# Optimization experiments

Hardware: AMD Instinct MI355X
Metric: run time of the kernel (lower is better)

The kernel has to match this reference:

```python
import jax, jax.numpy as jnp
import numpy as np

B, T_ENC, ENC_H = 32, 512, 512
H, E, V, STEPS = 512, 512, 32000, 64
EOS_IDX = 2


def setup_inputs() -> dict:
    key = jax.random.key(0)
    ks = jax.random.split(key, 20)
    s = 0.05
    inp = {
        "encoder_outputs": jax.random.normal(ks[0], (B, T_ENC, ENC_H), jnp.float32),
        "enc_h": jax.random.normal(ks[1], (1, B, ENC_H), jnp.float32),
        "enc_c": jax.random.normal(ks[2], (1, B, ENC_H), jnp.float32),
        "trg_var": jax.random.randint(ks[3], (B, STEPS), 0, V),
        "max_length": STEPS,
        # learned parameters
        "embedding": jax.random.normal(ks[4], (V, E), jnp.float32) * s,
        "Wa": jax.random.normal(ks[5], (T_ENC, E + H), jnp.float32) * s,   # attn: Linear(E+H -> T)
        "ba": jnp.zeros((T_ENC,), jnp.float32),
        "Wc": jax.random.normal(ks[6], (E, E + ENC_H), jnp.float32) * s,   # attn_combine
        "bc": jnp.zeros((E,), jnp.float32),
        "Wh0": jax.random.normal(ks[7], (H, ENC_H), jnp.float32) * s,      # enc_to_dec_h0 (no bias)
        "Wc0": jax.random.normal(ks[8], (H, ENC_H), jnp.float32) * s,      # enc_to_dec_c0 (no bias)
        "Wih": jax.random.normal(ks[9], (4 * H, E), jnp.float32) * s,      # LSTM input weights (i,f,g,o)
        "Whh": jax.random.normal(ks[10], (4 * H, H), jnp.float32) * s,
        "bih": jnp.zeros((4 * H,), jnp.float32),
        "bhh": jnp.zeros((4 * H,), jnp.float32),
        "Wp": jax.random.normal(ks[11], (H, E), jnp.float32) * s,          # pre_output_layer
        "bp": jnp.zeros((H,), jnp.float32),
        "Wo": jax.random.normal(ks[12], (V, H), jnp.float32) * s,          # output_layer
        "bo": jnp.zeros((V,), jnp.float32),
    }
    return inp


def _decode(encoder_outputs, enc_h, enc_c, embedding, Wa, ba, Wc, bc, Wh0, Wc0,
            Wih, Whh, bih, bhh, Wp, bp, Wo, bo, trg_var, max_length):
    # init hidden from encoder final state (pass_hidden_state, LSTM, 1 layer)
    h0 = enc_h[0] @ Wh0.T  # (B,H)
    c0 = enc_c[0] @ Wc0.T
    mask0 = jnp.ones((trg_var.shape[0],), bool)

    # teacher forcing: input embedding at step 0 is zeros, then emb(trg[:, i-1])
    emb_trg = embedding[trg_var[:, :max_length - 1]]          # (B,S-1,E)
    emb_seq = jnp.concatenate(
        [jnp.zeros((1,) + (trg_var.shape[0], embedding.shape[1]), embedding.dtype),
         jnp.transpose(emb_trg, (1, 0, 2))], axis=0)          # (S,B,E)

    def step(carry, emb_prev):
        h, c, mask = carry
        # Bahdanau-style location attention over encoder positions
        aw = jax.nn.softmax(jnp.concatenate([emb_prev, h], -1) @ Wa.T + ba, axis=-1)  # (B,T)
        ctx = jnp.einsum('bt,bte->be', aw, encoder_outputs)                            # (B,encH)
        comb = jax.nn.relu(jnp.concatenate([emb_prev, ctx], -1) @ Wc.T + bc)           # (B,E)
        # LSTM cell (PyTorch gate order i,f,g,o)
        gates = comb @ Wih.T + bih + h @ Whh.T + bhh
        i_, f_, g_, o_ = jnp.split(gates, 4, axis=-1)
        c = jax.nn.sigmoid(f_) * c + jax.nn.sigmoid(i_) * jnp.tanh(g_)
        h = jax.nn.sigmoid(o_) * jnp.tanh(c)
        # use_prev_word=False, use_dec_state=False -> predict from attn-combined output
        pre = comb @ Wp.T + bp                                                          # (B,H)
        lp = jax.nn.log_softmax(pre @ Wo.T + bo, axis=-1)                               # (B,V)
        pred = jnp.argmax(lp, axis=-1)
        mask_out = mask                       # masks are appended before the EOS update
        new_mask = (pred != EOS_IDX) & mask
        return (h, c, new_mask), (lp, pred, h, mask_out)

    (_, _, _), (lps, preds, states, masks) = jax.lax.scan(step, (h0, c0, mask0), emb_seq)
    return (jnp.transpose(lps, (1, 0, 2)),       # log_probs (B,S,V)
            preds.T,                              # preds (B,S)
            jnp.transpose(states, (1, 0, 2)),     # decoder states (B,S,H)
            masks.T.astype(jnp.int32))            # mask (B,S)


def reference(encoder_outputs, enc_h, enc_c, trg_var, max_length, embedding, Wa, ba,
              Wc, bc, Wh0, Wc0, Wih, Whh, bih, bhh, Wp, bp, Wo, bo):
    return _decode(encoder_outputs, enc_h, enc_c, embedding, Wa, ba, Wc, bc, Wh0, Wc0,
                   Wih, Whh, bih, bhh, Wp, bp, Wo, bo, trg_var, max_length)
```

## Files before the change

### kernel.cpp

```cpp
#include <hip/hip_runtime.h>


#define NEGF (-3.4028235e38f)

typedef short bf8 __attribute__((ext_vector_type(8)));
typedef unsigned short us8 __attribute__((ext_vector_type(8)));
typedef float f32x4 __attribute__((ext_vector_type(4)));

static __device__ __forceinline__ float sigf(float x) { return 1.0f / (1.0f + expf(-x)); }

static __device__ __forceinline__ float aload(const float* p) {
    return __hip_atomic_load(p, __ATOMIC_RELAXED, __HIP_MEMORY_SCOPE_AGENT);
}
static __device__ __forceinline__ void astore(float* p, float v) {
    __hip_atomic_store(p, v, __ATOMIC_RELAXED, __HIP_MEMORY_SCOPE_AGENT);
}
static __device__ __forceinline__ unsigned fordkey(float f) {
    unsigned u = __float_as_uint(f);
    return (u & 0x80000000u) ? ~u : (u | 0x80000000u);
}
static __device__ __forceinline__ unsigned short f2bf(float x) {
    unsigned u = __float_as_uint(x);
    return (unsigned short)((u + 0x7FFFu + ((u >> 16) & 1u)) >> 16);
}
static __device__ __forceinline__ float bf2f(unsigned short b) {
    return __uint_as_float(((unsigned)b) << 16);
}

static __device__ __forceinline__ void bar_arrive(unsigned* ctr) {
    __syncthreads();
    if (threadIdx.x == 0) {
        asm volatile("s_waitcnt vmcnt(0)" ::: "memory");
        __hip_atomic_fetch_add(ctr, 1u, __ATOMIC_RELAXED, __HIP_MEMORY_SCOPE_AGENT);
    }
}
static __device__ __forceinline__ void bar_wait(unsigned* ctr, unsigned target) {
    if (threadIdx.x == 0) {
        while ((int)(__hip_atomic_load(ctr, __ATOMIC_RELAXED, __HIP_MEMORY_SCOPE_AGENT)
                     - target) < 0) {
            __builtin_amdgcn_s_sleep(1);
        }
    }
    __syncthreads();
}

__global__ __launch_bounds__(256) void k_transpose(const float* __restrict__ src,
    float* __restrict__ dst, int rows, int cols, int ld, int coff)
{
    __shared__ float tile[32][33];
    int c0 = blockIdx.x * 32, r0 = blockIdx.y * 32;
    int tx = threadIdx.x & 31, ty = threadIdx.x >> 5;
#pragma unroll
    for (int i = 0; i < 32; i += 8)
        tile[ty + i][tx] = src[(size_t)(r0 + ty + i) * ld + coff + c0 + tx];
    __syncthreads();
#pragma unroll
    for (int i = 0; i < 32; i += 8)
        dst[(size_t)(c0 + ty + i) * rows + r0 + tx] = tile[tx][ty + i];
}

__global__ __launch_bounds__(512) void k_init_state(const float* __restrict__ vec,
    const float* __restrict__ W, float* __restrict__ dst, float* __restrict__ dstT)
{
    int b = blockIdx.x, j = threadIdx.x;
    __shared__ float sv[512];
    sv[j] = vec[b * 512 + j];
    __syncthreads();
    const float* wr = W + (size_t)j * 512;
    float a0 = 0, a1 = 0, a2 = 0, a3 = 0;
#pragma unroll 4
    for (int k = 0; k < 512; k += 4) {
        float4 w = *reinterpret_cast<const float4*>(wr + k);
        a0 += sv[k] * w.x; a1 += sv[k + 1] * w.y;
        a2 += sv[k + 2] * w.z; a3 += sv[k + 3] * w.w;
    }
    float v = (a0 + a1) + (a2 + a3);
    if (dst) dst[b * 512 + j] = v;
    dstT[j * 32 + b] = v;
}

__global__ __launch_bounds__(256) void k_gather(const int* __restrict__ trg,
    const float* __restrict__ emb, float* __restrict__ eseq)
{
    int gid = blockIdx.x * 256 + threadIdx.x;
    int m = gid >> 7, e4 = gid & 127;
    int t = m >> 5, b = m & 31;
    float4 v = make_float4(0.f, 0.f, 0.f, 0.f);
    if (t > 0) {
        int row = trg[b * 64 + (t - 1)];
        v = *reinterpret_cast<const float4*>(emb + (size_t)row * 512 + e4 * 4);
    }
    *reinterpret_cast<float4*>(eseq + (size_t)m * 512 + e4 * 4) = v;
}

__global__ __launch_bounds__(256) void k_gemm_nt(const float* __restrict__ A, int lda,
    size_t strideA, const float* __restrict__ B, int ldb, const float* __restrict__ bias,
    float* __restrict__ C, size_t strideC, int N, int K)
{
    __shared__ float sA[32][260];
    __shared__ float sB[32][132];
    A += strideA * blockIdx.z;
    C += strideC * blockIdx.z;
    int tid = threadIdx.x;
    int m0 = blockIdx.x * 256, n0 = blockIdx.y * 128;
    int tx = tid & 15, ty = tid >> 4;
    float acc[16][8] = {};
    for (int k0 = 0; k0 < K; k0 += 32) {
#pragma unroll
        for (int i = 0; i < 8; ++i) {
            int f4 = tid + i * 256;
            int r = f4 >> 3, c4 = f4 & 7;
            float4 va = *reinterpret_cast<const float4*>(A + (size_t)(m0 + r) * lda + k0 + c4 * 4);
            sA[c4 * 4 + 0][r] = va.x; sA[c4 * 4 + 1][r] = va.y;
            sA[c4 * 4 + 2][r] = va.z; sA[c4 * 4 + 3][r] = va.w;
        }
#pragma unroll
        for (int i = 0; i < 4; ++i) {
            int f4 = tid + i * 256;
            int r = f4 >> 3, c4 = f4 & 7;
            float4 vb = *reinterpret_cast<const float4*>(B + (size_t)(n0 + r) * ldb + k0 + c4 * 4);
            sB[c4 * 4 + 0][r] = vb.x; sB[c4 * 4 + 1][r] = vb.y;
            sB[c4 * 4 + 2][r] = vb.z; sB[c4 * 4 + 3][r] = vb.w;
        }
        __syncthreads();
#pragma unroll 4
        for (int k = 0; k < 32; ++k) {
            float a[16], b[8];
            *reinterpret_cast<float4*>(&a[0])  = *reinterpret_cast<const float4*>(&sA[k][ty * 16]);
            *reinterpret_cast<float4*>(&a[4])  = *reinterpret_cast<const float4*>(&sA[k][ty * 16 + 4]);
            *reinterpret_cast<float4*>(&a[8])  = *reinterpret_cast<const float4*>(&sA[k][ty * 16 + 8]);
            *reinterpret_cast<float4*>(&a[12]) = *reinterpret_cast<const float4*>(&sA[k][ty * 16 + 12]);
            *reinterpret_cast<float4*>(&b[0]) = *reinterpret_cast<const float4*>(&sB[k][tx * 8]);
            *reinterpret_cast<float4*>(&b[4]) = *reinterpret_cast<const float4*>(&sB[k][tx * 8 + 4]);
#pragma unroll
            for (int i = 0; i < 16; ++i)
#pragma unroll
                for (int j = 0; j < 8; ++j)
                    acc[i][j] += a[i] * b[j];
        }
        __syncthreads();
    }
#pragma unroll
    for (int i = 0; i < 16; ++i) {
        int row = m0 + ty * 16 + i;
        float* cp = C + (size_t)row * N + n0 + tx * 8;
        float v[8];
#pragma unroll
        for (int j = 0; j < 8; ++j) v[j] = acc[i][j];
        if (bias) {
            const float* bb = bias + n0 + tx * 8;
#pragma unroll
            for (int j = 0; j < 8; ++j) v[j] += bb[j];
        }
        *reinterpret_cast<float4*>(cp) = make_float4(v[0], v[1], v[2], v[3]);
        *reinterpret_cast<float4*>(cp + 4) = make_float4(v[4], v[5], v[6], v[7]);
    }
}

__global__ __launch_bounds__(256) void k_splitA(const float* __restrict__ pre,
    unsigned short* __restrict__ Asp)
{
    int idx = blockIdx.x * 256 + threadIdx.x;
    int m = idx >> 9, k = idx & 511;
    float x = pre[(size_t)m * 512 + k];
    unsigned short h = f2bf(x);
    unsigned short lo = f2bf(x - bf2f(h));
    unsigned short* ap = Asp + (size_t)m * 1024 + k;
    ap[0] = h; ap[512] = lo;
}

__global__ __launch_bounds__(256) void k_mfma(
    const unsigned short* __restrict__ Asp,
    const float* __restrict__ Wo,
    const float* __restrict__ bo,
    float* __restrict__ out0,
    unsigned long long* __restrict__ keyr, float* __restrict__ sumr)
{
    __shared__ unsigned short sAb[2][128 * 64];
    __shared__ unsigned short sBb[128 * 64];
    int tid = threadIdx.x;
    int m0 = blockIdx.x * 128, n0 = blockIdx.y * 128;
    int l = tid & 63, wv = tid >> 6;
    int wr = wv >> 1, wc = wv & 1;
    int lm = l & 15, lg = l >> 4;

    f32x4 acc[4][4] = {};

    for (int kb = 0; kb < 8; ++kb) {
#pragma unroll
        for (int i = 0; i < 8; ++i) {
            int p = tid + i * 256;
            int seg = p >> 10;
            int q2 = p & 1023;
            int row = q2 >> 3, pk = q2 & 7;
            int widx = row * 64 + ((pk * 8) ^ ((row & 7) << 3));
            *reinterpret_cast<us8*>(&sAb[seg][widx]) =
                *reinterpret_cast<const us8*>(
                    Asp + (size_t)(m0 + row) * 1024 + seg * 512 + kb * 64 + pk * 8);
        }
#pragma unroll
        for (int i = 0; i < 4; ++i) {
            int p = tid + i * 256;
            int row = p >> 3, pk = p & 7;
            int widx = row * 64 + ((pk * 8) ^ ((row & 7) << 3));
            const float* bp = Wo + (size_t)(n0 + row) * 512 + kb * 64 + pk * 8;
            float4 b0 = *reinterpret_cast<const float4*>(bp);
            float4 b1 = *reinterpret_cast<const float4*>(bp + 4);
            unsigned short hw[8] = { f2bf(b0.x), f2bf(b0.y), f2bf(b0.z), f2bf(b0.w),
                                     f2bf(b1.x), f2bf(b1.y), f2bf(b1.z), f2bf(b1.w) };
            *reinterpret_cast<us8*>(&sBb[widx]) = *reinterpret_cast<const us8*>(hw);
        }
        __syncthreads();
#pragma unroll
        for (int ks = 0; ks < 2; ++ks) {
            bf8 bfr[4];
#pragma unroll
            for (int fc = 0; fc < 4; ++fc) {
                int row = wc * 64 + fc * 16 + lm;
                int idx = row * 64 + ((ks * 32 + lg * 8) ^ ((row & 7) << 3));
                bfr[fc] = *reinterpret_cast<const bf8*>(&sBb[idx]);
            }
#pragma unroll
            for (int aseg = 0; aseg < 2; ++aseg) {
                bf8 af[4];
#pragma unroll
                for (int fr = 0; fr < 4; ++fr) {
                    int row = wr * 64 + fr * 16 + lm;
                    int idx = row * 64 + ((ks * 32 + lg * 8) ^ ((row & 7) << 3));
                    af[fr] = *reinterpret_cast<const bf8*>(&sAb[aseg][idx]);
                }
#pragma unroll
                for (int fr = 0; fr < 4; ++fr)
#pragma unroll
                    for (int fc = 0; fc < 4; ++fc)
                        acc[fr][fc] = __builtin_amdgcn_mfma_f32_16x16x32_bf16(
                            af[fr], bfr[fc], acc[fr][fc], 0, 0, 0);
            }
        }
        __syncthreads();
    }

#pragma unroll
    for (int fr = 0; fr < 4; ++fr) {
#pragma unroll
        for (int j = 0; j < 4; ++j) {
            int m = m0 + wr * 64 + fr * 16 + lg * 4 + j;
            size_t crow = (size_t)((m & 31) * 64 + (m >> 5));
            float* cp = out0 + crow * 32000 + n0 + wc * 64 + lm;
            float vv[4];
            float mval = NEGF; int midx = 0; float esum = 0.f;
#pragma unroll
            for (int fc = 0; fc < 4; ++fc) {
                int col = n0 + wc * 64 + fc * 16 + lm;
                float v = acc[fr][fc][j] + bo[col];
                vv[fc] = v;
                if (v > mval) { mval = v; midx = col; }
                esum += expf(v);
            }
#pragma unroll
            for (int fc = 0; fc < 4; ++fc) cp[fc * 16] = vv[fc];
#pragma unroll
            for (int msk = 1; msk <= 8; msk <<= 1) {
                float vo = __shfl_xor(mval, msk);
                int   io = __shfl_xor(midx, msk);
                float so = __shfl_xor(esum, msk);
                esum += so;
                if (vo > mval || (vo == mval && io < midx)) { mval = vo; midx = io; }
            }
            if (lm == 0) {
                unsigned long long key =
                    ((unsigned long long)fordkey(mval) << 32) | (unsigned)(~(unsigned)midx);
                atomicMax(&keyr[crow], key);
                atomicAdd(&sumr[crow], esum);
            }
        }
    }
}

__global__ __launch_bounds__(1024) void k_fused(
    const float* __restrict__ WaT, const float* __restrict__ zemb,
    const float* __restrict__ cemb, const float* __restrict__ encWc,
    const float* __restrict__ Wih, const float* __restrict__ Whh,
    const float* __restrict__ bih, const float* __restrict__ bhh,
    float* __restrict__ h_g, const float* __restrict__ cT,
    float* __restrict__ z_g, float* __restrict__ combS,
    float* __restrict__ comb_g, float* __restrict__ states,
    unsigned* __restrict__ bar)
{
    __shared__ float eW[512][64];
    __shared__ float hsh[512];
    __shared__ float csh[512];
    __shared__ float zl[512];
    __shared__ float red16[16][64];
    __shared__ float wred[8];
    __shared__ float wred2[8];
    __shared__ float sgate[4][64];
    __shared__ float carr[64];

    int tid = threadIdx.x, bid = blockIdx.x;
    int b = bid >> 3, s = bid & 7;
    int jj = tid & 63, q = tid >> 6;
    unsigned* barb = bar + b * 32;
    unsigned nbar = 0;

    int wv = tid >> 6, lane = tid & 63;
    int rowid = wv * 16 + (lane >> 2);
    int g = rowid >> 6, jgl = rowid & 63;
    int kq = lane & 3;
    const float* whp = Whh + (size_t)(g * 512 + s * 64 + jgl) * 512;
    const float* wip = Wih + (size_t)(g * 512 + s * 64 + jgl) * 512;

    {
        const float* src = encWc + ((size_t)b << 18) + s * 64;
        for (int i = tid; i < 512 * 16; i += 1024) {
            int t = i >> 4, c4 = i & 15;
            float4 v = *reinterpret_cast<const float4*>(src + (size_t)t * 512 + c4 * 4);
            *reinterpret_cast<float4*>(&eW[t][c4 * 4]) = v;
        }
    }
    if (tid < 64) carr[tid] = cT[(s * 64 + tid) * 32 + b];

    for (int tstep = 0; tstep < 64; ++tstep) {
        if (tid < 512) hsh[tid] = aload(h_g + b * 512 + tid);
        __syncthreads();
        {
            float acc = 0.f;
            const float* hp = hsh + q * 32;
            const float* wp = WaT + (size_t)(q * 32) * 512 + s * 64 + jj;
#pragma unroll 8
            for (int k = 0; k < 32; ++k)
                acc += hp[k] * wp[(size_t)k * 512];
            red16[q][jj] = acc;
        }
        __syncthreads();
        if (tid < 64) {
            float v = 0.f;
#pragma unroll
            for (int r = 0; r < 16; ++r) v += red16[r][jj];
            v += zemb[((size_t)tstep * 32 + b) * 512 + s * 64 + jj];
            astore(z_g + b * 512 + s * 64 + jj, v);
        }
        ++nbar; bar_arrive(barb);

        float acc_hh = 0.f;
#pragma unroll 8
        for (int i = 0; i < 32; ++i) {
            int k = kq * 4 + i * 16;
            float4 v4 = *reinterpret_cast<const float4*>(whp + k);
            acc_hh += v4.x * hsh[k]     + v4.y * hsh[k + 1]
                    + v4.z * hsh[k + 2] + v4.w * hsh[k + 3];
        }
        bar_wait(barb, nbar * 8u);

        {
            float zv = 0.f;
            if (tid < 512) {
                zv = aload(z_g + b * 512 + tid);
                float m = zv;
#pragma unroll
                for (int o = 32; o > 0; o >>= 1) m = fmaxf(m, __shfl_xor(m, o));
                if ((tid & 63) == 0) wred[tid >> 6] = m;
            }
            __syncthreads();
            float mx = fmaxf(fmaxf(fmaxf(wred[0], wred[1]), fmaxf(wred[2], wred[3])),
                             fmaxf(fmaxf(wred[4], wred[5]), fmaxf(wred[6], wred[7])));
            if (tid < 512) {
                float e = expf(zv - mx);
                zl[tid] = e;
                float sm = e;
#pragma unroll
                for (int o = 32; o > 0; o >>= 1) sm += __shfl_xor(sm, o);
                if ((tid & 63) == 0) wred2[tid >> 6] = sm;
            }
            __syncthreads();
            float ssum = ((wred2[0] + wred2[1]) + (wred2[2] + wred2[3]))
                       + ((wred2[4] + wred2[5]) + (wred2[6] + wred2[7]));
            float inv = 1.0f / ssum;

            float acc = 0.f;
#pragma unroll 8
            for (int i = 0; i < 32; ++i)
                acc += zl[q * 32 + i] * eW[q * 32 + i][jj];
            red16[q][jj] = acc;
            __syncthreads();
            if (tid < 64) {
                float v = 0.f;
#pragma unroll
                for (int r = 0; r < 16; ++r) v += red16[r][jj];
                v = v * inv + cemb[((size_t)tstep * 32 + b) * 512 + s * 64 + jj];
                v = fmaxf(v, 0.f);
                comb_g[((size_t)tstep * 32 + b) * 512 + s * 64 + jj] = v;
                astore(combS + b * 512 + s * 64 + jj, v);
            }
        }
        ++nbar; bar_arrive(barb); bar_wait(barb, nbar * 8u);

        if (tid < 512) csh[tid] = aload(combS + b * 512 + tid);
        __syncthreads();
        {
            float acc = acc_hh;
#pragma unroll 8
            for (int i = 0; i < 32; ++i) {
                int k = kq * 4 + i * 16;
                float4 w4 = *reinterpret_cast<const float4*>(wip + k);
                acc += w4.x * csh[k]     + w4.y * csh[k + 1]
                     + w4.z * csh[k + 2] + w4.w * csh[k + 3];
            }
            acc += __shfl_xor(acc, 1);
            acc += __shfl_xor(acc, 2);
            if (kq == 0) sgate[g][jgl] = acc;
        }
        __syncthreads();
        if (tid < 64) {
            int jg = s * 64 + tid;
            float gi = sgate[0][tid] + bih[jg] + bhh[jg];
            float gf = sgate[1][tid] + bih[512 + jg] + bhh[512 + jg];
            float gg = sgate[2][tid] + bih[1024 + jg] + bhh[1024 + jg];
            float go = sgate[3][tid] + bih[1536 + jg] + bhh[1536 + jg];
            float c = carr[tid];
            float cn = sigf(gf) * c + sigf(gi) * tanhf(gg);
            float hn = sigf(go) * tanhf(cn);
            carr[tid] = cn;
            astore(h_g + b * 512 + jg, hn);
            states[((size_t)b * 64 + tstep) * 512 + jg] = hn;
        }
        ++nbar; bar_arrive(barb); bar_wait(barb, nbar * 8u);
    }
}

__global__ __launch_bounds__(1024) void k_stepA(
    const float* __restrict__ WaT, const float* __restrict__ zemb_t,
    const float* __restrict__ cemb_t, const float* __restrict__ encWc,
    const float* __restrict__ h_g, float* __restrict__ comb_t,
    float* __restrict__ combT)
{
    int b = blockIdx.x, tid = threadIdx.x;
    int j = tid & 511, kh = tid >> 9;
    __shared__ float sh[512];
    __shared__ float zp[2][512];
    __shared__ float p[512];
    __shared__ float red[16];
    __shared__ float red2[16];

    if (tid < 512) sh[tid] = h_g[b * 512 + tid];
    __syncthreads();
    {
        float acc = 0.f;
        const float* hp = sh + kh * 256;
        const float* wp = WaT + (size_t)(kh * 256) * 512 + j;
#pragma unroll 4
        for (int k = 0; k < 256; ++k) acc += hp[k] * wp[(size_t)k * 512];
        zp[kh][j] = acc;
    }
    __syncthreads();
    float zv = 0.f;
    if (tid < 512) zv = zp[0][tid] + zp[1][tid] + zemb_t[b * 512 + tid];
    float m = (tid < 512) ? zv : NEGF;
#pragma unroll
    for (int o = 32; o > 0; o >>= 1) m = fmaxf(m, __shfl_xor(m, o));
    if ((tid & 63) == 0) red[tid >> 6] = m;
    __syncthreads();
    float mx = red[0];
#pragma unroll
    for (int w = 1; w < 16; ++w) mx = fmaxf(mx, red[w]);
    float e = (tid < 512) ? expf(zv - mx) : 0.f;
    float sm = e;
#pragma unroll
    for (int o = 32; o > 0; o >>= 1) sm += __shfl_xor(sm, o);
    if ((tid & 63) == 0) red2[tid >> 6] = sm;
    __syncthreads();
    float S = 0.f;
#pragma unroll
    for (int w = 0; w < 16; ++w) S += red2[w];
    if (tid < 512) p[tid] = e * (1.0f / S);
    __syncthreads();
    {
        float acc = 0.f;
        const float* pp = p + kh * 256;
        const float* ep = encWc + ((size_t)b << 18) + (size_t)(kh * 256) * 512 + j;
#pragma unroll 4
        for (int k = 0; k < 256; ++k) acc += pp[k] * ep[(size_t)k * 512];
        zp[kh][j] = acc;
    }
    __syncthreads();
    if (tid < 512) {
        float v = zp[0][tid] + zp[1][tid] + cemb_t[b * 512 + tid];
        v = fmaxf(v, 0.f);
        comb_t[b * 512 + tid] = v;
        combT[tid * 32 + b] = v;
    }
}

__global__ __launch_bounds__(512) void k_stepB(
    const float* __restrict__ Wih, const float* __restrict__ Whh,
    const float* __restrict__ bih, const float* __restrict__ bhh,
    const float* __restrict__ combT, const float* __restrict__ hTr,
    float* __restrict__ hTw, float* __restrict__ cT, float* __restrict__ h_g,
    float* __restrict__ states, int tstep)
{
    __shared__ float sg2[2][2][4][32];
    int tid = threadIdx.x, bid = blockIdx.x;
    {
        int bb = tid & 31, g = (tid >> 5) & 3, hf = (tid >> 7) & 1, j2 = tid >> 8;
        int jg = bid * 2 + j2;
        int grow = g * 512 + jg;
        const float* wi = Wih + (size_t)grow * 512 + hf * 256;
        const float* wh = Whh + (size_t)grow * 512 + hf * 256;
        const float* cb = combT + (size_t)hf * 256 * 32 + bb;
        const float* hb = hTr + (size_t)hf * 256 * 32 + bb;
        float acc = 0.f;
#pragma unroll 4
        for (int k4 = 0; k4 < 64; ++k4) {
            float4 wi4 = *reinterpret_cast<const float4*>(wi + k4 * 4);
            float4 wh4 = *reinterpret_cast<const float4*>(wh + k4 * 4);
            acc += wi4.x * cb[(k4 * 4 + 0) * 32] + wh4.x * hb[(k4 * 4 + 0) * 32];
            acc += wi4.y * cb[(k4 * 4 + 1) * 32] + wh4.y * hb[(k4 * 4 + 1) * 32];
            acc += wi4.z * cb[(k4 * 4 + 2) * 32] + wh4.z * hb[(k4 * 4 + 2) * 32];
            acc += wi4.w * cb[(k4 * 4 + 3) * 32] + wh4.w * hb[(k4 * 4 + 3) * 32];
        }
        sg2[hf][j2][g][bb] = acc;
    }
    __syncthreads();
    if (tid < 64) {
        int bb = tid & 31, j2 = tid >> 5;
        int jg = bid * 2 + j2;
        float gi = sg2[0][j2][0][bb] + sg2[1][j2][0][bb] + bih[jg] + bhh[jg];
        float gf = sg2[0][j2][1][bb] + sg2[1][j2][1][bb] + bih[512 + jg] + bhh[512 + jg];
        float gg = sg2[0][j2][2][bb] + sg2[1][j2][2][bb] + bih[1024 + jg] + bhh[1024 + jg];
        float go = sg2[0][j2][3][bb] + sg2[1][j2][3][bb] + bih[1536 + jg] + bhh[1536 + jg];
        float c = cT[jg * 32 + bb];
        float cn = sigf(gf) * c + sigf(gi) * tanhf(gg);
        float hn = sigf(go) * tanhf(cn);
        cT[jg * 32 + bb] = cn;
        hTw[jg * 32 + bb] = hn;
        h_g[bb * 512 + jg] = hn;
        states[((size_t)bb * 64 + tstep) * 512 + jg] = hn;
    }
}

__global__ __launch_bounds__(256) void k_finalize(float* __restrict__ out0,
    const unsigned long long* __restrict__ keyr, const float* __restrict__ sumr,
    const float* __restrict__ pre, const float* __restrict__ Wo,
    const float* __restrict__ bo, float* __restrict__ preds)
{
    int r = blockIdx.x, tid = threadIdx.x;
    float lse = logf(sumr[r]);
    unsigned k2 = (unsigned)(keyr[r] >> 32);
    float topv = __uint_as_float((k2 & 0x80000000u) ? (k2 ^ 0x80000000u) : ~k2);
    float thr = topv - 0.01f;

    __shared__ int cand[32];
    __shared__ float cex[32];
    __shared__ int ncand;
    if (tid == 0) ncand = 0;
    __syncthreads();

    float4* row4 = reinterpret_cast<float4*>(out0 + (size_t)r * 32000);
    for (int i = tid; i < 8000; i += 256) {
        float4 v = row4[i];
        if (v.x >= thr) { int p = atomicAdd(&ncand, 1); if (p < 32) cand[p] = i * 4; }
        if (v.y >= thr) { int p = atomicAdd(&ncand, 1); if (p < 32) cand[p] = i * 4 + 1; }
        if (v.z >= thr) { int p = atomicAdd(&ncand, 1); if (p < 32) cand[p] = i * 4 + 2; }
        if (v.w >= thr) { int p = atomicAdd(&ncand, 1); if (p < 32) cand[p] = i * 4 + 3; }
        v.x -= lse; v.y -= lse; v.z -= lse; v.w -= lse;
        row4[i] = v;
    }
    __syncthreads();
    int nc = min(ncand, 32);
    int m = (r & 63) * 32 + (r >> 6);
    const float* ap = pre + (size_t)m * 512;
    int w = tid >> 6, l = tid & 63;
    for (int c = w; c < nc; c += 4) {
        const float* wp = Wo + (size_t)cand[c] * 512;
        float d = 0.f;
#pragma unroll
        for (int e = 0; e < 8; ++e) d += ap[l * 8 + e] * wp[l * 8 + e];
#pragma unroll
        for (int o = 32; o > 0; o >>= 1) d += __shfl_xor(d, o);
        if (l == 0) cex[c] = d + bo[cand[c]];
    }
    __syncthreads();
    if (tid == 0) {
        float bv = NEGF; int bi = 0x7fffffff;
        for (int c = 0; c < nc; ++c) {
            float e = cex[c]; int ix = cand[c];
            if (e > bv || (e == bv && ix < bi)) { bv = e; bi = ix; }
        }
        preds[r] = (float)bi;
    }
}

__global__ __launch_bounds__(64) void k_masks(const float* __restrict__ preds,
    float* __restrict__ masks)
{
    int b = threadIdx.x;
    if (b < 32) {
        float mask = 1.0f;
        for (int t = 0; t < 64; ++t) {
            masks[b * 64 + t] = mask;
            if (preds[b * 64 + t] == 2.0f) mask = 0.0f;
        }
    }
}

extern "C" void kernel_launch(void* const* d_in, const int* in_sizes, int n_in,
                              void* d_out, int out_size, void* d_ws, size_t ws_size,
                              hipStream_t stream)
{
    (void)in_sizes; (void)n_in; (void)out_size; (void)ws_size;
    const float* enc  = (const float*)d_in[0];
    const float* ench = (const float*)d_in[1];
    const float* encc = (const float*)d_in[2];
    const int*   trg  = (const int*)d_in[3];
    const float* emb  = (const float*)d_in[5];
    const float* Wa   = (const float*)d_in[6];
    const float* ba   = (const float*)d_in[7];
    const float* Wc   = (const float*)d_in[8];
    const float* bc   = (const float*)d_in[9];
    const float* Wh0  = (const float*)d_in[10];
    const float* Wc0  = (const float*)d_in[11];
    const float* Wih  = (const float*)d_in[12];
    const float* Whh  = (const float*)d_in[13];
    const float* bih  = (const float*)d_in[14];
    const float* bhh  = (const float*)d_in[15];
    const float* Wp   = (const float*)d_in[16];
    const float* bp   = (const float*)d_in[17];
    const float* Wo   = (const float*)d_in[18];
    const float* bo   = (const float*)d_in[19];

    float* ws = (float*)d_ws;
    float* WaT   = ws;
    float* eseq  = ws + 262144;
    float* zemb  = ws + 1310720;
    float* cemb  = ws + 2359296;
    float* comb  = ws + 3407872;
    float* pre   = ws + 4456448;
    float* h_g   = ws + 5505024;
    float* hT0   = ws + 5521408;
    float* hT1   = ws + 5537792;
    float* cT    = ws + 5554176;
    float* z_g   = ws + 5570560;
    float* combS = ws + 5586944;
    unsigned* bar = (unsigned*)(ws + 5603328);
    unsigned long long* keyr = (unsigned long long*)(ws + 5604352);
    float* sumr  = ws + 5608448;
    unsigned short* Asp = (unsigned short*)(ws + 5610496);

    float* out0 = (float*)d_out;
    float* out1 = out0 + 65536000ull;
    float* out2 = out1 + 2048;
    float* out3 = out2 + 1048576;

    float* encWcB = out0;

    k_transpose<<<dim3(16, 16), 256, 0, stream>>>(Wa, WaT, 512, 512, 1024, 512);
    k_init_state<<<32, 512, 0, stream>>>(ench, Wh0, h_g, hT0);
    k_init_state<<<32, 512, 0, stream>>>(encc, Wc0, nullptr, cT);
    k_gather<<<1024, 256, 0, stream>>>(trg, emb, eseq);
    k_gemm_nt<<<dim3(8, 4, 1), 256, 0, stream>>>(eseq, 512, 0, Wa, 1024, ba, zemb, 0, 512, 512);
    k_gemm_nt<<<dim3(8, 4, 1), 256, 0, stream>>>(eseq, 512, 0, Wc, 1024, bc, cemb, 0, 512, 512);
    k_gemm_nt<<<dim3(2, 4, 32), 256, 0, stream>>>(enc, 512, (size_t)262144, Wc + 512, 1024,
                                                  nullptr, encWcB, (size_t)262144, 512, 512);
    hipMemsetAsync(bar, 0, 4096, stream);
    hipMemsetAsync(keyr, 0, 2048 * 8 + 2048 * 4, stream);

    {
        const float* a0 = WaT;  const float* a1 = zemb; const float* a2 = cemb;
        const float* a3 = encWcB; const float* a4 = Wih; const float* a5 = Whh;
        const float* a6 = bih;  const float* a7 = bhh;
        float* a8 = h_g;  const float* a9 = cT; float* a10 = z_g; float* a11 = combS;
        float* a12 = comb; float* a13 = out2;
        unsigned* a14 = bar;
        void* args[] = { &a0,&a1,&a2,&a3,&a4,&a5,&a6,&a7,&a8,&a9,&a10,&a11,
                         &a12,&a13,&a14 };
        hipError_t e = hipLaunchCooperativeKernel((const void*)k_fused, dim3(256), dim3(1024),
                                                  args, 0, stream);
        if (e != hipSuccess) {
            (void)hipGetLastError();
            for (int t = 0; t < 64; ++t) {
                k_stepA<<<32, 1024, 0, stream>>>(WaT, zemb + (size_t)t * 32 * 512,
                                                 cemb + (size_t)t * 32 * 512, encWcB, h_g,
                                                 comb + (size_t)t * 32 * 512, combS);
                const float* hTr = (t & 1) ? hT1 : hT0;
                float*       hTw = (t & 1) ? hT0 : hT1;
                k_stepB<<<256, 512, 0, stream>>>(Wih, Whh, bih, bhh, combS, hTr, hTw, cT,
                                                 h_g, out2, t);
            }
        }
    }

    k_gemm_nt<<<dim3(8, 4, 1), 256, 0, stream>>>(comb, 512, 0, Wp, 512, bp, pre, 0, 512, 512);
    k_splitA<<<4096, 256, 0, stream>>>(pre, Asp);
    k_mfma<<<dim3(16, 250), 256, 0, stream>>>(Asp, Wo, bo, out0, keyr, sumr);
    k_finalize<<<2048, 256, 0, stream>>>(out0, keyr, sumr, pre, Wo, bo, out1);
    k_masks<<<1, 64, 0, stream>>>(out1, out3);
}
```

Measured before the change: 1.967 ms.

## Use per-block flag barriers, prefetch Wih before wait, fuse bf16 split into GEMM

Replaces the counter-based fetch_add barrier among the 8 blocks of each batch row with per-block flag stores. Waiters poll all 8 flags with four 64-bit loads and proceed once every flag has reached the step value, which removes atomic RMW contention. Also prefetches the first quarter of the Wih row into registers before waiting on the barrier, so load latency overlaps the wait. Finally it folds the bf16 hi/lo split into the epilogue of the pre-output GEMM and drops the separate k_splitA launch. This adds register pressure and relies on the flag layout fitting 16 words per batch row.

```diff
diff --git a/kernel.cpp b/kernel.cpp
--- a/kernel.cpp
+++ b/kernel.cpp
@@ -27,17 +27,26 @@
     return __uint_as_float(((unsigned)b) << 16);
 }
 
-static __device__ __forceinline__ void bar_arrive(unsigned* ctr) {
+static __device__ __forceinline__ void bar_arrive(unsigned* flags, int s, unsigned val) {
     __syncthreads();
     if (threadIdx.x == 0) {
         asm volatile("s_waitcnt vmcnt(0)" ::: "memory");
-        __hip_atomic_fetch_add(ctr, 1u, __ATOMIC_RELAXED, __HIP_MEMORY_SCOPE_AGENT);
-    }
-}
-static __device__ __forceinline__ void bar_wait(unsigned* ctr, unsigned target) {
+        __hip_atomic_store(flags + s, val, __ATOMIC_RELAXED, __HIP_MEMORY_SCOPE_AGENT);
+    }
+}
+static __device__ __forceinline__ void bar_wait(unsigned* flags, unsigned val) {
     if (threadIdx.x == 0) {
-        while ((int)(__hip_atomic_load(ctr, __ATOMIC_RELAXED, __HIP_MEMORY_SCOPE_AGENT)
-                     - target) < 0) {
+        const unsigned long long* f64 = (const unsigned long long*)flags;
+        for (;;) {
+            unsigned long long a = __hip_atomic_load(f64 + 0, __ATOMIC_RELAXED, __HIP_MEMORY_SCOPE_AGENT);
+            unsigned long long b = __hip_atomic_load(f64 + 1, __ATOMIC_RELAXED, __HIP_MEMORY_SCOPE_AGENT);
+            unsigned long long c = __hip_atomic_load(f64 + 2, __ATOMIC_RELAXED, __HIP_MEMORY_SCOPE_AGENT);
+            unsigned long long d = __hip_atomic_load(f64 + 3, __ATOMIC_RELAXED, __HIP_MEMORY_SCOPE_AGENT);
+            unsigned m0 = min((unsigned)a, (unsigned)(a >> 32));
+            unsigned m1 = min((unsigned)b, (unsigned)(b >> 32));
+            unsigned m2 = min((unsigned)c, (unsigned)(c >> 32));
+            unsigned m3 = min((unsigned)d, (unsigned)(d >> 32));
+            if (min(min(m0, m1), min(m2, m3)) >= val) break;
             __builtin_amdgcn_s_sleep(1);
         }
     }
@@ -95,7 +104,7 @@
 
 __global__ __launch_bounds__(256) void k_gemm_nt(const float* __restrict__ A, int lda,
     size_t strideA, const float* __restrict__ B, int ldb, const float* __restrict__ bias,
-    float* __restrict__ C, size_t strideC, int N, int K)
+    float* __restrict__ C, size_t strideC, int N, int K, unsigned short* __restrict__ asp)
 {
     __shared__ float sA[32][260];
     __shared__ float sB[32][132];
@@ -154,19 +163,18 @@
         }
         *reinterpret_cast<float4*>(cp) = make_float4(v[0], v[1], v[2], v[3]);
         *reinterpret_cast<float4*>(cp + 4) = make_float4(v[4], v[5], v[6], v[7]);
-    }
-}
-
-__global__ __launch_bounds__(256) void k_splitA(const float* __restrict__ pre,
-    unsigned short* __restrict__ Asp)
-{
-    int idx = blockIdx.x * 256 + threadIdx.x;
-    int m = idx >> 9, k = idx & 511;
-    float x = pre[(size_t)m * 512 + k];
-    unsigned short h = f2bf(x);
-    unsigned short lo = f2bf(x - bf2f(h));
-    unsigned short* ap = Asp + (size_t)m * 1024 + k;
-    ap[0] = h; ap[512] = lo;
+        if (asp) {
+            unsigned short hi[8], lo[8];
+#pragma unroll
+            for (int j = 0; j < 8; ++j) {
+                hi[j] = f2bf(v[j]);
+                lo[j] = f2bf(v[j] - bf2f(hi[j]));
+            }
+            unsigned short* ap = asp + (size_t)row * 1024 + n0 + tx * 8;
+            *reinterpret_cast<us8*>(ap)       = *reinterpret_cast<const us8*>(hi);
+            *reinterpret_cast<us8*>(ap + 512) = *reinterpret_cast<const us8*>(lo);
+        }
+    }
 }
 
 __global__ __launch_bounds__(256) void k_mfma(
@@ -300,7 +308,7 @@
     int tid = threadIdx.x, bid = blockIdx.x;
     int b = bid >> 3, s = bid & 7;
     int jj = tid & 63, q = tid >> 6;
-    unsigned* barb = bar + b * 32;
+    unsigned* barb = bar + b * 16;
     unsigned nbar = 0;
 
     int wv = tid >> 6, lane = tid & 63;
@@ -340,7 +348,7 @@
             v += zemb[((size_t)tstep * 32 + b) * 512 + s * 64 + jj];
             astore(z_g + b * 512 + s * 64 + jj, v);
         }
-        ++nbar; bar_arrive(barb);
+        ++nbar; bar_arrive(barb, s, nbar);
 
         float acc_hh = 0.f;
 #pragma unroll 8
@@ -350,7 +358,7 @@
             acc_hh += v4.x * hsh[k]     + v4.y * hsh[k + 1]
                     + v4.z * hsh[k + 2] + v4.w * hsh[k + 3];
         }
-        bar_wait(barb, nbar * 8u);
+        bar_wait(barb, nbar);
 
         {
             float zv = 0.f;
@@ -393,14 +401,27 @@
                 astore(combS + b * 512 + s * 64 + jj, v);
             }
         }
-        ++nbar; bar_arrive(barb); bar_wait(barb, nbar * 8u);
+        ++nbar; bar_arrive(barb, s, nbar);
+
+        float4 wpre[8];
+#pragma unroll
+        for (int i = 0; i < 8; ++i)
+            wpre[i] = *reinterpret_cast<const float4*>(wip + kq * 4 + i * 16);
+        bar_wait(barb, nbar);
 
         if (tid < 512) csh[tid] = aload(combS + b * 512 + tid);
         __syncthreads();
         {
             float acc = acc_hh;
+#pragma unroll
+            for (int i = 0; i < 8; ++i) {
+                int k = kq * 4 + i * 16;
+                float4 w4 = wpre[i];
+                acc += w4.x * csh[k]     + w4.y * csh[k + 1]
+                     + w4.z * csh[k + 2] + w4.w * csh[k + 3];
+            }
 #pragma unroll 8
-            for (int i = 0; i < 32; ++i) {
+            for (int i = 8; i < 32; ++i) {
                 int k = kq * 4 + i * 16;
                 float4 w4 = *reinterpret_cast<const float4*>(wip + k);
                 acc += w4.x * csh[k]     + w4.y * csh[k + 1]
@@ -424,7 +445,7 @@
             astore(h_g + b * 512 + jg, hn);
             states[((size_t)b * 64 + tstep) * 512 + jg] = hn;
         }
-        ++nbar; bar_arrive(barb); bar_wait(barb, nbar * 8u);
+        ++nbar; bar_arrive(barb, s, nbar); bar_wait(barb, nbar);
     }
 }
 
@@ -657,11 +678,11 @@
     k_init_state<<<32, 512, 0, stream>>>(ench, Wh0, h_g, hT0);
     k_init_state<<<32, 512, 0, stream>>>(encc, Wc0, nullptr, cT);
     k_gather<<<1024, 256, 0, stream>>>(trg, emb, eseq);
-    k_gemm_nt<<<dim3(8, 4, 1), 256, 0, stream>>>(eseq, 512, 0, Wa, 1024, ba, zemb, 0, 512, 512);
-    k_gemm_nt<<<dim3(8, 4, 1), 256, 0, stream>>>(eseq, 512, 0, Wc, 1024, bc, cemb, 0, 512, 512);
+    k_gemm_nt<<<dim3(8, 4, 1), 256, 0, stream>>>(eseq, 512, 0, Wa, 1024, ba, zemb, 0, 512, 512, nullptr);
+    k_gemm_nt<<<dim3(8, 4, 1), 256, 0, stream>>>(eseq, 512, 0, Wc, 1024, bc, cemb, 0, 512, 512, nullptr);
     k_gemm_nt<<<dim3(2, 4, 32), 256, 0, stream>>>(enc, 512, (size_t)262144, Wc + 512, 1024,
-                                                  nullptr, encWcB, (size_t)262144, 512, 512);
-    hipMemsetAsync(bar, 0, 4096, stream);
+                                                  nullptr, encWcB, (size_t)262144, 512, 512, nullptr);
+    hipMemsetAsync(bar, 0, 2048, stream);
     hipMemsetAsync(keyr, 0, 2048 * 8 + 2048 * 4, stream);
 
     {
@@ -689,8 +710,7 @@
         }
     }
 
-    k_gemm_nt<<<dim3(8, 4, 1), 256, 0, stream>>>(comb, 512, 0, Wp, 512, bp, pre, 0, 512, 512);
-    k_splitA<<<4096, 256, 0, stream>>>(pre, Asp);
+    k_gemm_nt<<<dim3(8, 4, 1), 256, 0, stream>>>(comb, 512, 0, Wp, 512, bp, pre, 0, 512, 512, Asp);
     k_mfma<<<dim3(16, 250), 256, 0, stream>>>(Asp, Wo, bo, out0, keyr, sumr);
     k_finalize<<<2048, 256, 0, stream>>>(out0, keyr, sumr, pre, Wo, bo, out1);
     k_masks<<<1, 64, 0, stream>>>(out1, out3);
```

Measured after the change: 2.000 ms. About the same (+1.7%).

## Fuse bf16 split into pre GEMM and double M tile in output MFMA

Applied to the files above, without the earlier changes.

The separate k_splitA kernel is gone. The pre-output GEMM epilogue now writes the hi/lo bf16 split of its result straight into the Asp buffer. The vocab-projection MFMA kernel now uses 256-row M tiles instead of 128, so each Wo tile is loaded and converted to bf16 half as many times across the grid. The cost is twice the LDS for the A tile and twice the accumulator registers, which may lower occupancy, and only half as many blocks are launched.

```diff
diff --git a/kernel.cpp b/kernel.cpp
--- a/kernel.cpp
+++ b/kernel.cpp
@@ -95,7 +95,7 @@
 
 __global__ __launch_bounds__(256) void k_gemm_nt(const float* __restrict__ A, int lda,
     size_t strideA, const float* __restrict__ B, int ldb, const float* __restrict__ bias,
-    float* __restrict__ C, size_t strideC, int N, int K)
+    float* __restrict__ C, size_t strideC, int N, int K, unsigned short* __restrict__ asp)
 {
     __shared__ float sA[32][260];
     __shared__ float sB[32][132];
@@ -154,19 +154,18 @@
         }
         *reinterpret_cast<float4*>(cp) = make_float4(v[0], v[1], v[2], v[3]);
         *reinterpret_cast<float4*>(cp + 4) = make_float4(v[4], v[5], v[6], v[7]);
-    }
-}
-
-__global__ __launch_bounds__(256) void k_splitA(const float* __restrict__ pre,
-    unsigned short* __restrict__ Asp)
-{
-    int idx = blockIdx.x * 256 + threadIdx.x;
-    int m = idx >> 9, k = idx & 511;
-    float x = pre[(size_t)m * 512 + k];
-    unsigned short h = f2bf(x);
-    unsigned short lo = f2bf(x - bf2f(h));
-    unsigned short* ap = Asp + (size_t)m * 1024 + k;
-    ap[0] = h; ap[512] = lo;
+        if (asp) {
+            unsigned short hi[8], lo[8];
+#pragma unroll
+            for (int j = 0; j < 8; ++j) {
+                hi[j] = f2bf(v[j]);
+                lo[j] = f2bf(v[j] - bf2f(hi[j]));
+            }
+            unsigned short* ap = asp + (size_t)row * 1024 + n0 + tx * 8;
+            *reinterpret_cast<us8*>(ap)       = *reinterpret_cast<const us8*>(hi);
+            *reinterpret_cast<us8*>(ap + 512) = *reinterpret_cast<const us8*>(lo);
+        }
+    }
 }
 
 __global__ __launch_bounds__(256) void k_mfma(
@@ -176,22 +175,22 @@
     float* __restrict__ out0,
     unsigned long long* __restrict__ keyr, float* __restrict__ sumr)
 {
-    __shared__ unsigned short sAb[2][128 * 64];
+    __shared__ unsigned short sAb[2][256 * 64];
     __shared__ unsigned short sBb[128 * 64];
     int tid = threadIdx.x;
-    int m0 = blockIdx.x * 128, n0 = blockIdx.y * 128;
+    int m0 = blockIdx.x * 256, n0 = blockIdx.y * 128;
     int l = tid & 63, wv = tid >> 6;
     int wr = wv >> 1, wc = wv & 1;
     int lm = l & 15, lg = l >> 4;
 
-    f32x4 acc[4][4] = {};
+    f32x4 acc[2][4][4] = {};
 
     for (int kb = 0; kb < 8; ++kb) {
 #pragma unroll
-        for (int i = 0; i < 8; ++i) {
+        for (int i = 0; i < 16; ++i) {
             int p = tid + i * 256;
-            int seg = p >> 10;
-            int q2 = p & 1023;
+            int seg = p >> 11;
+            int q2 = p & 2047;
             int row = q2 >> 3, pk = q2 & 7;
             int widx = row * 64 + ((pk * 8) ^ ((row & 7) << 3));
             *reinterpret_cast<us8*>(&sAb[seg][widx]) =
@@ -221,57 +220,63 @@
                 bfr[fc] = *reinterpret_cast<const bf8*>(&sBb[idx]);
             }
 #pragma unroll
-            for (int aseg = 0; aseg < 2; ++aseg) {
-                bf8 af[4];
-#pragma unroll
-                for (int fr = 0; fr < 4; ++fr) {
-                    int row = wr * 64 + fr * 16 + lm;
-                    int idx = row * 64 + ((ks * 32 + lg * 8) ^ ((row & 7) << 3));
-                    af[fr] = *reinterpret_cast<const bf8*>(&sAb[aseg][idx]);
+            for (int mt = 0; mt < 2; ++mt) {
+#pragma unroll
+                for (int aseg = 0; aseg < 2; ++aseg) {
+                    bf8 af[4];
+#pragma unroll
+                    for (int fr = 0; fr < 4; ++fr) {
+                        int row = mt * 128 + wr * 64 + fr * 16 + lm;
+                        int idx = row * 64 + ((ks * 32 + lg * 8) ^ ((row & 7) << 3));
+                        af[fr] = *reinterpret_cast<const bf8*>(&sAb[aseg][idx]);
+                    }
+#pragma unroll
+                    for (int fr = 0; fr < 4; ++fr)
+#pragma unroll
+                        for (int fc = 0; fc < 4; ++fc)
+                            acc[mt][fr][fc] = __builtin_amdgcn_mfma_f32_16x16x32_bf16(
+                                af[fr], bfr[fc], acc[mt][fr][fc], 0, 0, 0);
                 }
-#pragma unroll
-                for (int fr = 0; fr < 4; ++fr)
-#pragma unroll
-                    for (int fc = 0; fc < 4; ++fc)
-                        acc[fr][fc] = __builtin_amdgcn_mfma_f32_16x16x32_bf16(
-                            af[fr], bfr[fc], acc[fr][fc], 0, 0, 0);
             }
         }
         __syncthreads();
     }
 
 #pragma unroll
-    for (int fr = 0; fr < 4; ++fr) {
-#pragma unroll
-        for (int j = 0; j < 4; ++j) {
-            int m = m0 + wr * 64 + fr * 16 + lg * 4 + j;
-            size_t crow = (size_t)((m & 31) * 64 + (m >> 5));
-            float* cp = out0 + crow * 32000 + n0 + wc * 64 + lm;
-            float vv[4];
-            float mval = NEGF; int midx = 0; float esum = 0.f;
-#pragma unroll
-            for (int fc = 0; fc < 4; ++fc) {
-                int col = n0 + wc * 64 + fc * 16 + lm;
-                float v = acc[fr][fc][j] + bo[col];
-                vv[fc] = v;
-                if (v > mval) { mval = v; midx = col; }
-                esum += expf(v);
-            }
-#pragma unroll
-            for (int fc = 0; fc < 4; ++fc) cp[fc * 16] = vv[fc];
-#pragma unroll
-            for (int msk = 1; msk <= 8; msk <<= 1) {
-                float vo = __shfl_xor(mval, msk);
-                int   io = __shfl_xor(midx, msk);
-                float so = __shfl_xor(esum, msk);
-                esum += so;
-                if (vo > mval || (vo == mval && io < midx)) { mval = vo; midx = io; }
-            }
-            if (lm == 0) {
-                unsigned long long key =
-                    ((unsigned long long)fordkey(mval) << 32) | (unsigned)(~(unsigned)midx);
-                atomicMax(&keyr[crow], key);
-                atomicAdd(&sumr[crow], esum);
+    for (int mt = 0; mt < 2; ++mt) {
+#pragma unroll
+        for (int fr = 0; fr < 4; ++fr) {
+#pragma unroll
+            for (int j = 0; j < 4; ++j) {
+                int m = m0 + mt * 128 + wr * 64 + fr * 16 + lg * 4 + j;
+                size_t crow = (size_t)((m & 31) * 64 + (m >> 5));
+                float* cp = out0 + crow * 32000 + n0 + wc * 64 + lm;
+                float vv[4];
+                float mval = NEGF; int midx = 0; float esum = 0.f;
+#pragma unroll
+                for (int fc = 0; fc < 4; ++fc) {
+                    int col = n0 + wc * 64 + fc * 16 + lm;
+                    float v = acc[mt][fr][fc][j] + bo[col];
+                    vv[fc] = v;
+                    if (v > mval) { mval = v; midx = col; }
+                    esum += expf(v);
+                }
+#pragma unroll
+                for (int fc = 0; fc < 4; ++fc) cp[fc * 16] = vv[fc];
+#pragma unroll
+                for (int msk = 1; msk <= 8; msk <<= 1) {
+                    float vo = __shfl_xor(mval, msk);
+                    int   io = __shfl_xor(midx, msk);
+                    float so = __shfl_xor(esum, msk);
+                    esum += so;
+                    if (vo > mval || (vo == mval && io < midx)) { mval = vo; midx = io; }
+                }
+                if (lm == 0) {
+                    unsigned long long key =
+                        ((unsigned long long)fordkey(mval) << 32) | (unsigned)(~(unsigned)midx);
+                    atomicMax(&keyr[crow], key);
+                    atomicAdd(&sumr[crow], esum);
+                }
             }
         }
     }
@@ -657,10 +662,10 @@
     k_init_state<<<32, 512, 0, stream>>>(ench, Wh0, h_g, hT0);
     k_init_state<<<32, 512, 0, stream>>>(encc, Wc0, nullptr, cT);
     k_gather<<<1024, 256, 0, stream>>>(trg, emb, eseq);
-    k_gemm_nt<<<dim3(8, 4, 1), 256, 0, stream>>>(eseq, 512, 0, Wa, 1024, ba, zemb, 0, 512, 512);
-    k_gemm_nt<<<dim3(8, 4, 1), 256, 0, stream>>>(eseq, 512, 0, Wc, 1024, bc, cemb, 0, 512, 512);
+    k_gemm_nt<<<dim3(8, 4, 1), 256, 0, stream>>>(eseq, 512, 0, Wa, 1024, ba, zemb, 0, 512, 512, nullptr);
+    k_gemm_nt<<<dim3(8, 4, 1), 256, 0, stream>>>(eseq, 512, 0, Wc, 1024, bc, cemb, 0, 512, 512, nullptr);
     k_gemm_nt<<<dim3(2, 4, 32), 256, 0, stream>>>(enc, 512, (size_t)262144, Wc + 512, 1024,
-                                                  nullptr, encWcB, (size_t)262144, 512, 512);
+                                                  nullptr, encWcB, (size_t)262144, 512, 512, nullptr);
     hipMemsetAsync(bar, 0, 4096, stream);
     hipMemsetAsync(keyr, 0, 2048 * 8 + 2048 * 4, stream);
 
@@ -689,9 +694,8 @@
         }
     }
 
-    k_gemm_nt<<<dim3(8, 4, 1), 256, 0, stream>>>(comb, 512, 0, Wp, 512, bp, pre, 0, 512, 512);
-    k_splitA<<<4096, 256, 0, stream>>>(pre, Asp);
-    k_mfma<<<dim3(16, 250), 256, 0, stream>>>(Asp, Wo, bo, out0, keyr, sumr);
+    k_gemm_nt<<<dim3(8, 4, 1), 256, 0, stream>>>(comb, 512, 0, Wp, 512, bp, pre, 0, 512, 512, Asp);
+    k_mfma<<<dim3(8, 250), 256, 0, stream>>>(Asp, Wo, bo, out0, keyr, sumr);
     k_finalize<<<2048, 256, 0, stream>>>(out0, keyr, sumr, pre, Wo, bo, out1);
     k_masks<<<1, 64, 0, stream>>>(out1, out3);
 }
```

Result: slower. 2.049 ms (+4.2%).
